# Kernel optimization log

Measured on AMD Instinct MI355X. Metric: run time of the kernel, lower is better.

Reference implementation:

```python
import jax, jax.numpy as jnp
import numpy as np

N, E, IN, HID, OUT = 20000, 640000, 128, 64, 32


def setup_inputs() -> dict:
    key = jax.random.key(0)
    ks = jax.random.split(key, 20)
    nrm = lambda k, sh, s: jax.random.normal(k, sh, jnp.float32) * s
    return {
        "x": nrm(ks[0], (N, IN), 1.0),
        "edge_index": jax.random.randint(ks[1], (2, E), 0, N, dtype=jnp.int32),
        "edge_attr": nrm(ks[2], (E, 1), 1.0),
        # GAT layer 1 (in->hid)
        "W1": nrm(ks[3], (IN, HID), 1.0 / np.sqrt(IN)),
        "a1_src": nrm(ks[4], (HID,), 1.0 / np.sqrt(HID)),
        "a1_dst": nrm(ks[5], (HID,), 1.0 / np.sqrt(HID)),
        "b1": jnp.zeros((HID,), jnp.float32),
        # GAT layer 2 (hid->32)
        "W2": nrm(ks[6], (HID, OUT), 1.0 / np.sqrt(HID)),
        "a2_src": nrm(ks[7], (OUT,), 1.0 / np.sqrt(OUT)),
        "a2_dst": nrm(ks[8], (OUT,), 1.0 / np.sqrt(OUT)),
        "b2": jnp.zeros((OUT,), jnp.float32),
        # LSTM(32,32): gates ordered i,f,g,o as in torch
        "W_ih": nrm(ks[9], (4 * OUT, OUT), 1.0 / np.sqrt(OUT)),
        "W_hh": nrm(ks[10], (4 * OUT, OUT), 1.0 / np.sqrt(OUT)),
        "b_ih": jnp.zeros((4 * OUT,), jnp.float32),
        "b_hh": jnp.zeros((4 * OUT,), jnp.float32),
        # fc1: ReLU -> Linear(32,1)
        "fc1_w": nrm(ks[11], (1, OUT), 1.0 / np.sqrt(OUT)),
        "fc1_b": jnp.zeros((1,), jnp.float32),
        # fc2: Linear(32,16) -> ReLU -> Linear(16,1) -> Sigmoid
        "fc2_w1": nrm(ks[12], (16, OUT), 1.0 / np.sqrt(OUT)),
        "fc2_b1": jnp.zeros((16,), jnp.float32),
        "fc2_w2": nrm(ks[13], (1, 16), 1.0 / np.sqrt(16)),
        "fc2_b2": jnp.zeros((1,), jnp.float32),
    }


def gat_layer(x, src, dst, W, a_src, a_dst, b, n):
    # PyG GATConv (1 head, default): h = xW; e_ij = LeakyReLU(a_src.h_j + a_dst.h_i)
    h = x @ W                              # [n, F]
    es = h @ a_src                          # [n] source scores
    ed = h @ a_dst                          # [n] target scores
    e = jax.nn.leaky_relu(es[src] + ed[dst], 0.2)   # [E']
    m = jax.ops.segment_max(e, dst, num_segments=n)
    p = jnp.exp(e - m[dst])
    denom = jax.ops.segment_sum(p, dst, num_segments=n)
    alpha = p / denom[dst]                  # segment softmax over in-edges of dst
    out = jax.ops.segment_sum(alpha[:, None] * h[src], dst, num_segments=n)
    return out + b


def reference(x, edge_index, edge_attr, W1, a1_src, a1_dst, b1, W2, a2_src,
              a2_dst, b2, W_ih, W_hh, b_ih, b_hh, fc1_w, fc1_b, fc2_w1,
              fc2_b1, fc2_w2, fc2_b2):
    n = x.shape[0]
    # GATConv default add_self_loops=True
    loop = jnp.arange(n, dtype=edge_index.dtype)
    src = jnp.concatenate([edge_index[0], loop])
    dst = jnp.concatenate([edge_index[1], loop])
    # edge_attr unused: GATConv has edge_dim=None
    feats = jax.nn.relu(gat_layer(x, src, dst, W1, a1_src, a1_dst, b1, n))
    feats = gat_layer(feats, src, dst, W2, a2_src, a2_dst, b2, n)   # [n, 32]

    # classification head on mean-pooled features
    x_c = jnp.mean(feats, axis=0)
    x_c = jax.nn.sigmoid(jax.nn.relu(x_c @ fc2_w1.T + fc2_b1) @ fc2_w2.T + fc2_b2)  # (1,)

    # LSTM over node sequence (unbatched, seq_len=n); take final cell state c_n
    def cell(carry, x_t):
        h, c = carry
        z = x_t @ W_ih.T + b_ih + h @ W_hh.T + b_hh
        i, f, g, o = jnp.split(z, 4)
        c = jax.nn.sigmoid(f) * c + jax.nn.sigmoid(i) * jnp.tanh(g)
        h = jax.nn.sigmoid(o) * jnp.tanh(c)
        return (h, c), None

    init = (jnp.zeros((OUT,), feats.dtype), jnp.zeros((OUT,), feats.dtype))
    (h_n, c_n), _ = jax.lax.scan(cell, init, feats)
    x_r = jax.nn.relu(c_n) @ fc1_w.T + fc1_b   # (1,)

    return jnp.stack([x_c, x_r], axis=0)       # (2, 1)
```

## Files before the change

kernel.cpp:

```cpp
#include <hip/hip_runtime.h>

#define IN_F 128
#define HID_F 64
#define OUT_F 32
#define ENC_NEG_INF 0x007FFFFFu
#define LOG2E 1.44269504088896340736f

#define OFF_OUT1   0
#define OFF_OUT2   1280000
#define OFF_D1     1920000
#define OFF_D2     1940000
#define OFF_SUM    1960000
#define ZERO_FLOATS 1960064
#define OFF_M1     1960064
#define OFF_M2     1980064
#define OFF_H1     2000064
#define OFF_H2     3280064
#define OFF_ES1    3920064
#define OFF_ED1    3940064
#define OFF_ES2    3960064
#define OFF_ED2    3980064
#define OFF_EBUF   4000064
#define OFF_ZX     4660064

__device__ __forceinline__ unsigned enc_f(float f) {
  unsigned b = __float_as_uint(f);
  return (b & 0x80000000u) ? ~b : (b | 0x80000000u);
}
__device__ __forceinline__ float dec_f(unsigned u) {
  unsigned b = (u & 0x80000000u) ? (u & 0x7FFFFFFFu) : ~u;
  return __uint_as_float(b);
}

template <int CTRL>
__device__ __forceinline__ float qperm(float x) {
  return __uint_as_float((unsigned)__builtin_amdgcn_update_dpp(
      0, (int)__float_as_uint(x), CTRL, 0xF, 0xF, true));
}

__global__ void k_initm(unsigned* __restrict__ m1, unsigned* __restrict__ m2, int n) {
  int i = blockIdx.x * blockDim.x + threadIdx.x;
  if (i < n) { m1[i] = ENC_NEG_INF; m2[i] = ENC_NEG_INF; }
}

__global__ void k_gemm1(const float* __restrict__ x, const float* __restrict__ W1,
                        const float* __restrict__ a_src, const float* __restrict__ a_dst,
                        float* __restrict__ h1, float* __restrict__ es, float* __restrict__ ed) {
  int n = blockIdx.x;
  int f = threadIdx.x;
  const float* xr = x + n * IN_F;
  float acc = 0.f;
#pragma unroll 8
  for (int k = 0; k < IN_F; ++k) acc = fmaf(xr[k], W1[k * HID_F + f], acc);
  h1[n * HID_F + f] = acc;
  float s = acc * a_src[f];
  float d = acc * a_dst[f];
#pragma unroll
  for (int off = 32; off; off >>= 1) {
    s += __shfl_down(s, off, 64);
    d += __shfl_down(d, off, 64);
  }
  if (f == 0) { es[n] = s; ed[n] = d; }
}

__global__ void k_emax(const int* __restrict__ ei, const float* __restrict__ es,
                       const float* __restrict__ ed, float* __restrict__ ebuf,
                       unsigned* __restrict__ menc, int E, int EP) {
  int i = blockIdx.x * blockDim.x + threadIdx.x;
  if (i >= EP) return;
  int src, dst;
  if (i < E) { src = ei[i]; dst = ei[E + i]; } else { src = dst = i - E; }
  float e = es[src] + ed[dst];
  e = (e >= 0.f) ? e : 0.2f * e;
  ebuf[i] = e;
  atomicMax(&menc[dst], enc_f(e));
}

__global__ void k_ep(const int* __restrict__ ei, float* __restrict__ ebuf,
                     const unsigned* __restrict__ menc, float* __restrict__ denom,
                     int E, int EP) {
  int i = blockIdx.x * blockDim.x + threadIdx.x;
  if (i >= EP) return;
  int dst = (i < E) ? ei[E + i] : (i - E);
  float p = __expf(ebuf[i] - dec_f(menc[dst]));
  ebuf[i] = p;
  atomicAdd(&denom[dst], p);
}

template <int F>
__global__ void k_aggr(const int* __restrict__ ei, const float* __restrict__ ebuf,
                       const float* __restrict__ denom, const float* __restrict__ h,
                       float* __restrict__ out, int E, int EP) {
  int gt = blockIdx.x * blockDim.x + threadIdx.x;
  int lane = gt % F;
  int e = gt / F;
  if (e >= EP) return;
  int src, dst;
  if (e < E) { src = ei[e]; dst = ei[E + e]; } else { src = dst = e - E; }
  float alpha = ebuf[e] / denom[dst];
  atomicAdd(&out[dst * F + lane], alpha * h[src * F + lane]);
}

__global__ void k_gemm2(const float* __restrict__ out1, const float* __restrict__ b1,
                        const float* __restrict__ W2, const float* __restrict__ a_src,
                        const float* __restrict__ a_dst, float* __restrict__ h2,
                        float* __restrict__ es, float* __restrict__ ed, int N) {
  int lane = threadIdx.x;
  int f = lane & 31;
  int n = blockIdx.x * 2 + (lane >> 5);
  if (n >= N) return;
  const float* r = out1 + n * HID_F;
  float acc = 0.f;
#pragma unroll 8
  for (int k = 0; k < HID_F; ++k) {
    float v = r[k] + b1[k];
    v = v > 0.f ? v : 0.f;
    acc = fmaf(v, W2[k * OUT_F + f], acc);
  }
  h2[n * OUT_F + f] = acc;
  float s = acc * a_src[f];
  float d = acc * a_dst[f];
#pragma unroll
  for (int off = 16; off; off >>= 1) {
    s += __shfl_down(s, off, 32);
    d += __shfl_down(d, off, 32);
  }
  if (f == 0) { es[n] = s; ed[n] = d; }
}

__global__ void k_zx(const float* __restrict__ out2, const float* __restrict__ b2,
                     const float* __restrict__ Wih, const float* __restrict__ bih,
                     const float* __restrict__ bhh, float* __restrict__ Zx) {
  int r = threadIdx.x;
  int t = blockIdx.x;
  const float* xr = out2 + t * OUT_F;
  float acc = bih[r] + bhh[r];
#pragma unroll
  for (int k = 0; k < OUT_F; ++k) acc = fmaf(xr[k] + b2[k], Wih[r * OUT_F + k], acc);
  float scl = (r >= 64 && r < 96) ? 2.f * LOG2E : LOG2E;
  int pos = ((r & 31) << 2) | (((r >> 5) & 1) << 1) | (r >> 6);
  Zx[t * 128 + pos] = acc * scl;
}

__global__ void k_mean(const float* __restrict__ out2, const float* __restrict__ b2,
                       float* __restrict__ sum, int N) {
  int k = threadIdx.x & 31;
  int row = threadIdx.x >> 5;
  float acc = 0.f;
  for (int n = blockIdx.x * 8 + row; n < N; n += gridDim.x * 8)
    acc += out2[n * OUT_F + k] + b2[k];
  __shared__ float s[256];
  s[threadIdx.x] = acc;
  __syncthreads();
  if (threadIdx.x < 32) {
    float tot = 0.f;
#pragma unroll
    for (int j = 0; j < 8; ++j) tot += s[j * 32 + k];
    atomicAdd(&sum[k], tot);
  }
}

__global__ void k_head(const float* __restrict__ sum, const float* __restrict__ w1,
                       const float* __restrict__ bb1, const float* __restrict__ w2,
                       const float* __restrict__ bb2, float* __restrict__ out, float invN) {
  if (threadIdx.x == 0 && blockIdx.x == 0) {
    float xc[32];
#pragma unroll
    for (int k = 0; k < 32; ++k) xc[k] = sum[k] * invN;
    float t2 = bb2[0];
    for (int j = 0; j < 16; ++j) {
      float a = bb1[j];
#pragma unroll
      for (int k = 0; k < 32; ++k) a = fmaf(w1[j * 32 + k], xc[k], a);
      a = a > 0.f ? a : 0.f;
      t2 = fmaf(w2[j], a, t2);
    }
    out[0] = 1.f / (1.f + __expf(-t2));
  }
}

__global__ void __launch_bounds__(64, 1) k_lstm(
    const float* __restrict__ Zx, const float* __restrict__ Whh,
    const float* __restrict__ fc1w, const float* __restrict__ fc1b,
    float* __restrict__ out, int N) {
  const int l = threadIdx.x;
  const int j = l >> 1;
  const int p = l & 1;
  const int rowA = p * 32 + j;
  const int rowB = (2 + p) * 32 + j;
  const float sclA = LOG2E;
  const float sclB = p ? LOG2E : 2.f * LOG2E;

  float wA[32], wB[32];
#pragma unroll
  for (int k = 0; k < 32; ++k) {
    wA[k] = Whh[rowA * 32 + k] * sclA;
    wB[k] = Whh[rowB * 32 + k] * sclB;
  }

  const float2* pz = (const float2*)Zx + l;
  float2 zr[8];
#pragma unroll
  for (int s = 0; s < 8; ++s) zr[s] = pz[s * 64];

  const float n2L = -2.f * LOG2E;
  float h = 0.f, c = 0.f;
  for (int t = 0; t < N; t += 8) {
#pragma unroll
    for (int s = 0; s < 8; ++s) {
      float zA = zr[s].x, zB = zr[s].y;
      zr[s] = pz[(t + s + 8) * 64];
      unsigned hbits = __float_as_uint(h);
#pragma unroll
      for (int k = 0; k < 32; ++k) {
        float hk = __uint_as_float(__builtin_amdgcn_readlane(hbits, 2 * k));
        zA = fmaf(wA[k], hk, zA);
        zB = fmaf(wB[k], hk, zB);
      }
      float sA = __builtin_amdgcn_rcpf(1.f + exp2f(-zA));
      float sB = __builtin_amdgcn_rcpf(1.f + exp2f(-zB));
      float fgx = qperm<0xB1>(sA);
      float ogx = qperm<0xB1>(sB);
      float gg = fmaf(2.f, sB, -1.f);
      c = fmaf(fgx, c, sA * gg);
      float r3 = __builtin_amdgcn_rcpf(1.f + exp2f(n2L * c));
      float tc = fmaf(2.f, r3, -1.f);
      h = ogx * tc;
    }
  }

  float v = (p == 0) ? fmaxf(c, 0.f) * fc1w[j] : 0.f;
#pragma unroll
  for (int off = 32; off; off >>= 1) v += __shfl_down(v, off, 64);
  if (l == 0) out[1] = v + fc1b[0];
}

extern "C" void kernel_launch(void* const* d_in, const int* in_sizes, int n_in,
                              void* d_out, int out_size, void* d_ws, size_t ws_size,
                              hipStream_t stream) {
  const float* x    = (const float*)d_in[0];
  const int*   ei   = (const int*)d_in[1];
  const float* W1   = (const float*)d_in[3];
  const float* a1s  = (const float*)d_in[4];
  const float* a1d  = (const float*)d_in[5];
  const float* b1   = (const float*)d_in[6];
  const float* W2   = (const float*)d_in[7];
  const float* a2s  = (const float*)d_in[8];
  const float* a2d  = (const float*)d_in[9];
  const float* b2   = (const float*)d_in[10];
  const float* Wih  = (const float*)d_in[11];
  const float* Whh  = (const float*)d_in[12];
  const float* bih  = (const float*)d_in[13];
  const float* bhh  = (const float*)d_in[14];
  const float* fc1w = (const float*)d_in[15];
  const float* fc1b = (const float*)d_in[16];
  const float* f2w1 = (const float*)d_in[17];
  const float* f2b1 = (const float*)d_in[18];
  const float* f2w2 = (const float*)d_in[19];
  const float* f2b2 = (const float*)d_in[20];

  const int N  = in_sizes[0] / IN_F;
  const int E  = in_sizes[1] / 2;
  const int EP = E + N;

  float* ws = (float*)d_ws;
  float*    out1  = ws + OFF_OUT1;
  float*    out2  = ws + OFF_OUT2;
  float*    d1    = ws + OFF_D1;
  float*    d2    = ws + OFF_D2;
  float*    sum   = ws + OFF_SUM;
  unsigned* m1    = (unsigned*)(ws + OFF_M1);
  unsigned* m2    = (unsigned*)(ws + OFF_M2);
  float*    h1    = ws + OFF_H1;
  float*    h2    = ws + OFF_H2;
  float*    es1   = ws + OFF_ES1;
  float*    ed1   = ws + OFF_ED1;
  float*    es2   = ws + OFF_ES2;
  float*    ed2   = ws + OFF_ED2;
  float*    ebuf  = ws + OFF_EBUF;
  float*    Zx    = ws + OFF_ZX;

  hipMemsetAsync(d_ws, 0, (size_t)ZERO_FLOATS * 4, stream);
  k_initm<<<(N + 255) / 256, 256, 0, stream>>>(m1, m2, N);

  k_gemm1<<<N, 64, 0, stream>>>(x, W1, a1s, a1d, h1, es1, ed1);
  int eb = (EP + 255) / 256;
  k_emax<<<eb, 256, 0, stream>>>(ei, es1, ed1, ebuf, m1, E, EP);
  k_ep<<<eb, 256, 0, stream>>>(ei, ebuf, m1, d1, E, EP);
  k_aggr<64><<<((size_t)EP * 64 + 255) / 256, 256, 0, stream>>>(ei, ebuf, d1, h1, out1, E, EP);

  k_gemm2<<<(N + 1) / 2, 64, 0, stream>>>(out1, b1, W2, a2s, a2d, h2, es2, ed2, N);
  k_emax<<<eb, 256, 0, stream>>>(ei, es2, ed2, ebuf, m2, E, EP);
  k_ep<<<eb, 256, 0, stream>>>(ei, ebuf, m2, d2, E, EP);
  k_aggr<32><<<((size_t)EP * 32 + 255) / 256, 256, 0, stream>>>(ei, ebuf, d2, h2, out2, E, EP);

  k_zx<<<N, 128, 0, stream>>>(out2, b2, Wih, bih, bhh, Zx);
  k_mean<<<64, 256, 0, stream>>>(out2, b2, sum, N);
  k_head<<<1, 64, 0, stream>>>(sum, f2w1, f2b1, f2w2, f2b2, (float*)d_out, 1.f / (float)N);
  k_lstm<<<1, 64, 0, stream>>>(Zx, Whh, fc1w, fc1b, (float*)d_out, N);
}
```

Baseline: 5.743 ms.

## Broadcast LSTM hidden state via LDS double buffer and use packed FMAs

Result: faster. 5.332 ms (-7.2%).

```diff
diff --git a/kernel.cpp b/kernel.cpp
--- a/kernel.cpp
+++ b/kernel.cpp
@@ -5,6 +5,13 @@
 #define OUT_F 32
 #define ENC_NEG_INF 0x007FFFFFu
 #define LOG2E 1.44269504088896340736f
+
+typedef float f32x2 __attribute__((ext_vector_type(2)));
+
+#define PK_LO(acc, w, hs) \
+  asm("v_pk_fma_f32 %0, %1, %2, %0 op_sel_hi:[1,0,1]" : "+v"(acc) : "v"(w), "v"(hs))
+#define PK_HI(acc, w, hs) \
+  asm("v_pk_fma_f32 %0, %1, %2, %0 op_sel:[0,1,0]" : "+v"(acc) : "v"(w), "v"(hs))
 
 #define OFF_OUT1   0
 #define OFF_OUT2   1280000
@@ -191,32 +198,45 @@
   const float sclA = LOG2E;
   const float sclB = p ? LOG2E : 2.f * LOG2E;
 
-  float wA[32], wB[32];
+  f32x2 w2[32];
 #pragma unroll
   for (int k = 0; k < 32; ++k) {
-    wA[k] = Whh[rowA * 32 + k] * sclA;
-    wB[k] = Whh[rowB * 32 + k] * sclB;
-  }
+    f32x2 w;
+    w.x = Whh[rowA * 32 + k] * sclA;
+    w.y = Whh[rowB * 32 + k] * sclB;
+    w2[k] = w;
+  }
+
+  __shared__ float hb[2][64];
+  hb[1][l] = 0.f;
 
   const float2* pz = (const float2*)Zx + l;
-  float2 zr[8];
-#pragma unroll
-  for (int s = 0; s < 8; ++s) zr[s] = pz[s * 64];
+  f32x2 zr[8];
+#pragma unroll
+  for (int s = 0; s < 8; ++s) { float2 v = pz[s * 64]; zr[s].x = v.x; zr[s].y = v.y; }
 
   const float n2L = -2.f * LOG2E;
-  float h = 0.f, c = 0.f;
+  float c = 0.f;
   for (int t = 0; t < N; t += 8) {
 #pragma unroll
     for (int s = 0; s < 8; ++s) {
-      float zA = zr[s].x, zB = zr[s].y;
-      zr[s] = pz[(t + s + 8) * 64];
-      unsigned hbits = __float_as_uint(h);
-#pragma unroll
-      for (int k = 0; k < 32; ++k) {
-        float hk = __uint_as_float(__builtin_amdgcn_readlane(hbits, 2 * k));
-        zA = fmaf(wA[k], hk, zA);
-        zB = fmaf(wB[k], hk, zB);
+      const int u = t + s;
+      f32x2 acc0 = zr[s];
+      f32x2 acc1; acc1.x = 0.f; acc1.y = 0.f;
+      { float2 v = pz[(u + 8) * 64]; zr[s].x = v.x; zr[s].y = v.y; }
+      const f32x2* hbr = (const f32x2*)hb[(u + 1) & 1];
+      f32x2 hk2[16];
+#pragma unroll
+      for (int k2 = 0; k2 < 16; ++k2) hk2[k2] = hbr[k2];
+#pragma unroll
+      for (int q = 0; q < 8; ++q) {
+        PK_LO(acc0, w2[2 * q],      hk2[q]);
+        PK_LO(acc1, w2[16 + 2 * q], hk2[8 + q]);
+        PK_HI(acc0, w2[2 * q + 1],      hk2[q]);
+        PK_HI(acc1, w2[16 + 2 * q + 1], hk2[8 + q]);
       }
+      float zA = acc0.x + acc1.x;
+      float zB = acc0.y + acc1.y;
       float sA = __builtin_amdgcn_rcpf(1.f + exp2f(-zA));
       float sB = __builtin_amdgcn_rcpf(1.f + exp2f(-zB));
       float fgx = qperm<0xB1>(sA);
@@ -225,7 +245,8 @@
       c = fmaf(fgx, c, sA * gg);
       float r3 = __builtin_amdgcn_rcpf(1.f + exp2f(n2L * c));
       float tc = fmaf(2.f, r3, -1.f);
-      h = ogx * tc;
+      float h = ogx * tc;
+      hb[u & 1][p * 32 + j] = h;
     }
   }
 
```
